# Kernel tuning notes

Hardware: AMD Instinct MI355X
Metric: run time of the kernel (lower is better)

Reference implementation:

```python
import jax, jax.numpy as jnp
import numpy as np
from functools import partial

EPS = 1e-5
PATCH = 3
STYLE_STRENGTH = 1.0


def _whiten_color_mats(x):
    # x: (b, c, n) already flattened; returns mean, eigvecs, eigvals of covariance
    mean = x.mean(axis=-1, keepdims=True)
    xc = x - mean
    n = x.shape[-1]
    cov = jnp.einsum('bcn,bdn->bcd', xc, xc) / (n - 1)
    evals, evecs = jnp.linalg.eigh(cov)
    evals = jnp.maximum(evals, EPS)
    return mean, xc, evecs, evals


def whitening(x):
    b, c, h, w = x.shape
    xf = x.reshape(b, c, h * w)
    _, xc, E, d = _whiten_color_mats(xf)
    # W = E diag(d^-1/2) E^T
    Wm = jnp.einsum('bce,be,bde->bcd', E, d ** -0.5, E)
    return jnp.einsum('bcd,bdn->bcn', Wm, xc).reshape(b, c, h, w)


def coloring(x, style):
    b, c, h, w = x.shape
    xf = x.reshape(b, c, h * w)
    sf = style.reshape(b, c, -1)
    smean, sc, E, d = _whiten_color_mats(sf)
    Cm = jnp.einsum('bce,be,bde->bcd', E, d ** 0.5, E)
    out = jnp.einsum('bcd,bdn->bcn', Cm, xf) + smean
    return out.reshape(b, c, h, w)


def extract_style_kernels(style):
    # returns (b, hw, c, 3, 3) patches and (b, hw, 1, 1, 1) L2 norms
    b, c, H, W = style.shape
    p = jnp.pad(style, ((0, 0), (0, 0), (1, 1), (1, 1)), mode='reflect')
    patches = jnp.stack([p[:, :, i:i + H, j:j + W]
                         for i in range(PATCH) for j in range(PATCH)], axis=-1)  # (b,c,H,W,9)
    k = patches.reshape(b, c, H * W, PATCH * PATCH).transpose(0, 2, 1, 3)  # (b,hw,c,9)
    norm = jnp.sqrt(jnp.sum(k * k, axis=(2, 3))) + EPS  # (b,hw)
    return k.reshape(b, H * W, c, PATCH, PATCH), norm[:, :, None, None, None]


_DN = ('NCHW', 'OIHW', 'NCHW')


def _conv_per_sample(feat, kern):
    # feat (c,H,W), kern (o,c,3,3): reflect-pad 1, VALID conv -> (o,H,W)
    fp = jnp.pad(feat, ((0, 0), (1, 1), (1, 1)), mode='reflect')
    out = jax.lax.conv_general_dilated(fp[None], kern, (1, 1), 'VALID',
                                       dimension_numbers=_DN)
    return out[0]


def _deconv_per_sample(onehot, kern):
    # conv_transpose2d(stride=1, padding=2) == VALID conv with flipped, transposed kernel
    kt = jnp.flip(kern, axis=(-2, -1)).transpose(1, 0, 2, 3)  # (c, hw, 3, 3)
    fp = jnp.pad(onehot, ((0, 0), (1, 1), (1, 1)), mode='reflect')
    out = jax.lax.conv_general_dilated(fp[None], kt, (1, 1), 'VALID',
                                       dimension_numbers=_DN)
    return out[0]


def norm_deconvolution(h, w, patch_size):
    full = np.zeros((h + patch_size - 1, w + patch_size - 1), dtype=np.float32)
    for x in range(patch_size):
        for y in range(patch_size):
            full[y:y + h, x:x + w] += 1.0
    pw = (patch_size - 1) // 2
    if pw > 0:
        full = full[pw:-pw, pw:-pw]
    return jnp.asarray(full)[None, None]  # (1,1,h,w)


def reassemble_feature(nc, ns):
    b, c, H, W = nc.shape
    hw = H * W
    kern, norm = extract_style_kernels(ns)
    score = jax.vmap(_conv_per_sample)(nc, kern / norm)  # (b, hw, H, W)
    idx = jnp.argmax(score, axis=1)  # (b, H, W)
    onehot = (jnp.arange(hw, dtype=idx.dtype)[None, :, None, None] == idx[:, None]
              ).astype(nc.dtype)  # (b, hw, H, W)
    recon = jax.vmap(_deconv_per_sample)(onehot, kern)  # (b, c, H, W)
    return recon / norm_deconvolution(H, W, PATCH).astype(recon.dtype)


def setup_inputs() -> dict:
    key = jax.random.key(0)
    k1, k2 = jax.random.split(key)
    content_feature = jax.random.normal(k1, (2, 256, 64, 64), dtype=jnp.float32)
    style_feature = jax.random.normal(k2, (2, 256, 64, 64), dtype=jnp.float32)
    return {"content_feature": content_feature, "style_feature": style_feature}


def reference(content_feature, style_feature):
    nc = whitening(content_feature)
    ns = whitening(style_feature)
    reassembled = reassemble_feature(nc, ns)
    stylized = coloring(reassembled, style_feature)
    return (1.0 - STYLE_STRENGTH) * content_feature + STYLE_STRENGTH * stylized
```

## Files before the change

kernel.cpp:

```cpp
#include <hip/hip_runtime.h>
#include <hip/hip_bf16.h>

#define C_ 256
#define N_ 4096
#define CN (C_*N_)
#define EPSF 1e-5f
#define NS_ITERS 6
#define KSPLIT 16
#define LSTR 40

typedef _Float16 f16x8 __attribute__((ext_vector_type(8)));
typedef float f32x4 __attribute__((ext_vector_type(4)));

__device__ __forceinline__ int refl(int t) {
  return t < 0 ? -t : (t > 63 ? 126 - t : t);
}

__device__ __forceinline__ unsigned short f2h(float x) {
  _Float16 h = (_Float16)x;
  return __builtin_bit_cast(unsigned short, h);
}
__device__ __forceinline__ float h2f(unsigned short u) {
  return (float)__builtin_bit_cast(_Float16, u);
}

__device__ __forceinline__ void fma16(float acc[4][4], float a0, float a1, float a2, float a3, float4 b) {
  acc[0][0] += a0*b.x; acc[0][1] += a0*b.y; acc[0][2] += a0*b.z; acc[0][3] += a0*b.w;
  acc[1][0] += a1*b.x; acc[1][1] += a1*b.y; acc[1][2] += a1*b.z; acc[1][3] += a1*b.w;
  acc[2][0] += a2*b.x; acc[2][1] += a2*b.y; acc[2][2] += a2*b.z; acc[2][3] += a2*b.w;
  acc[3][0] += a3*b.x; acc[3][1] += a3*b.y; acc[3][2] += a3*b.z; acc[3][3] += a3*b.w;
}

__device__ __forceinline__ void mm64_3term(unsigned short* sm, const float* A, const float* B,
                                           int m0, int n0, f32x4 acc[2][2]) {
  const int P = 64*LSTR;
  int t = threadIdx.x;
  int lane = t & 63;
  int wv = (t >> 7) & 1, wu = (t >> 6) & 1;
  int lx16 = lane & 15, quad = lane >> 4;
  int srow = t >> 2, sseg = (t & 3) * 8;
#pragma unroll
  for (int i = 0; i < 2; i++)
#pragma unroll
    for (int j = 0; j < 2; j++) acc[i][j] = (f32x4){0.f, 0.f, 0.f, 0.f};
  for (int k0 = 0; k0 < 256; k0 += 32) {
    __syncthreads();
    {
      const float* pa = &A[(size_t)(m0 + srow)*256 + k0 + sseg];
      const float* pb = &B[(size_t)(n0 + srow)*256 + k0 + sseg];
#pragma unroll
      for (int g = 0; g < 2; g++) {
        float4 va = *(const float4*)(pa + g*4);
        float4 vb = *(const float4*)(pb + g*4);
        float fa[4] = {va.x, va.y, va.z, va.w};
        float fb[4] = {vb.x, vb.y, vb.z, vb.w};
        unsigned short ha[4], la[4], hb[4], lb[4];
#pragma unroll
        for (int j = 0; j < 4; j++) {
          unsigned short h = f2h(fa[j]); ha[j] = h; la[j] = f2h(fa[j] - h2f(h));
          h = f2h(fb[j]); hb[j] = h; lb[j] = f2h(fb[j] - h2f(h));
        }
        int lo_ = srow*LSTR + sseg + g*4;
        *(ushort4*)&sm[0*P + lo_] = make_ushort4(ha[0], ha[1], ha[2], ha[3]);
        *(ushort4*)&sm[1*P + lo_] = make_ushort4(la[0], la[1], la[2], la[3]);
        *(ushort4*)&sm[2*P + lo_] = make_ushort4(hb[0], hb[1], hb[2], hb[3]);
        *(ushort4*)&sm[3*P + lo_] = make_ushort4(lb[0], lb[1], lb[2], lb[3]);
      }
    }
    __syncthreads();
    f16x8 ah[2], al[2], bh[2], bl[2];
#pragma unroll
    for (int mt = 0; mt < 2; mt++) {
      int arow = (wv*32 + mt*16 + lx16)*LSTR + quad*8;
      ah[mt] = *(const f16x8*)&sm[0*P + arow];
      al[mt] = *(const f16x8*)&sm[1*P + arow];
    }
#pragma unroll
    for (int nt = 0; nt < 2; nt++) {
      int brow = (wu*32 + nt*16 + lx16)*LSTR + quad*8;
      bh[nt] = *(const f16x8*)&sm[2*P + brow];
      bl[nt] = *(const f16x8*)&sm[3*P + brow];
    }
#pragma unroll
    for (int mt = 0; mt < 2; mt++)
#pragma unroll
      for (int nt = 0; nt < 2; nt++) {
        f32x4 a = acc[mt][nt];
        a = __builtin_amdgcn_mfma_f32_16x16x32_f16(ah[mt], bh[nt], a, 0, 0, 0);
        a = __builtin_amdgcn_mfma_f32_16x16x32_f16(ah[mt], bl[nt], a, 0, 0, 0);
        a = __builtin_amdgcn_mfma_f32_16x16x32_f16(al[mt], bh[nt], a, 0, 0, 0);
        acc[mt][nt] = a;
      }
  }
}

__global__ __launch_bounds__(256) void k_mean(const float* content, const float* style,
                                              float* means) {
  int c = blockIdx.x, m = blockIdx.y, t = threadIdx.x;
  const float* x = (m < 2 ? content : style) + (size_t)(m & 1) * CN + (size_t)c * N_;
  float s = 0.f;
  for (int i = t; i < N_; i += 256) s += x[i];
  __shared__ float red[256];
  red[t] = s; __syncthreads();
  for (int off = 128; off > 0; off >>= 1) { if (t < off) red[t] += red[t + off]; __syncthreads(); }
  if (t == 0) means[m * C_ + c] = red[0] * (1.f / N_);
}

__global__ __launch_bounds__(256) void k_splitcov(const float* content, const float* style,
                                                  unsigned short* sp) {
  int m = blockIdx.y;
  const float* x = (m < 2 ? content : style) + (size_t)(m & 1) * CN;
  size_t base = (size_t)m * 2 * (size_t)CN;
  size_t i = ((size_t)blockIdx.x * 256 + threadIdx.x) * 4;
  float4 v = *(const float4*)&x[i];
  float vv[4] = {v.x, v.y, v.z, v.w};
  unsigned short h[4], lo[4];
#pragma unroll
  for (int j = 0; j < 4; j++) {
    unsigned short hh = f2h(vv[j]);
    float r1 = vv[j] - h2f(hh);
    h[j] = hh; lo[j] = f2h(r1);
  }
  *(ushort4*)&sp[base + i]      = make_ushort4(h[0], h[1], h[2], h[3]);
  *(ushort4*)&sp[base + CN + i] = make_ushort4(lo[0], lo[1], lo[2], lo[3]);
}

__global__ __launch_bounds__(512) void k_covmm(const unsigned short* sp, float* covp) {
  __shared__ unsigned short sm[4*128*LSTR];
  const int P = 128*LSTR;
  int t = threadIdx.x;
  int kc = blockIdx.x, m = blockIdx.z;
  int ti = blockIdx.y >> 1, tj = blockIdx.y & 1;
  const unsigned short* Xh = sp + (size_t)m * 2 * (size_t)CN;
  const unsigned short* Xl = Xh + CN;
  int v0 = ti * 128, u0 = tj * 128;
  int wave = t >> 6, lane = t & 63;
  int wv = wave >> 1, wu = wave & 1;
  int lx16 = lane & 15, quad = lane >> 4;
  int srow = t >> 2, sseg = (t & 3) * 8;
  f32x4 acc[2][4];
#pragma unroll
  for (int i = 0; i < 2; i++)
#pragma unroll
    for (int j = 0; j < 4; j++) acc[i][j] = (f32x4){0.f, 0.f, 0.f, 0.f};

  int kbeg = kc * (N_ / KSPLIT), kend = kbeg + (N_ / KSPLIT);
  for (int k0 = kbeg; k0 < kend; k0 += 32) {
    __syncthreads();
    {
      size_t goA = (size_t)(v0 + srow) * N_ + k0 + sseg;
      size_t goB = (size_t)(u0 + srow) * N_ + k0 + sseg;
      int lo_ = srow * LSTR + sseg;
      *(float4*)&sm[0*P + lo_] = *(const float4*)&Xh[goA];
      *(float4*)&sm[1*P + lo_] = *(const float4*)&Xl[goA];
      *(float4*)&sm[2*P + lo_] = *(const float4*)&Xh[goB];
      *(float4*)&sm[3*P + lo_] = *(const float4*)&Xl[goB];
    }
    __syncthreads();
#pragma unroll
    for (int mt = 0; mt < 2; mt++) {
      int arow = (wv*32 + mt*16 + lx16)*LSTR + quad*8;
      f16x8 ah = *(const f16x8*)&sm[0*P + arow];
      f16x8 al = *(const f16x8*)&sm[1*P + arow];
#pragma unroll
      for (int nt = 0; nt < 4; nt++) {
        int brow = (wu*64 + nt*16 + lx16)*LSTR + quad*8;
        f16x8 bh = *(const f16x8*)&sm[2*P + brow];
        f16x8 bl = *(const f16x8*)&sm[3*P + brow];
        f32x4 a = acc[mt][nt];
        a = __builtin_amdgcn_mfma_f32_16x16x32_f16(ah, bh, a, 0, 0, 0);
        a = __builtin_amdgcn_mfma_f32_16x16x32_f16(ah, bl, a, 0, 0, 0);
        a = __builtin_amdgcn_mfma_f32_16x16x32_f16(al, bh, a, 0, 0, 0);
        acc[mt][nt] = a;
      }
    }
  }
  float* O = covp + ((size_t)kc*4 + m) * 65536;
#pragma unroll
  for (int mt = 0; mt < 2; mt++)
#pragma unroll
    for (int nt = 0; nt < 4; nt++)
#pragma unroll
      for (int i = 0; i < 4; i++)
        O[(size_t)(v0 + wv*32 + mt*16 + quad*4 + i)*C_ + (u0 + wu*64 + nt*16 + lx16)] =
            acc[mt][nt][i];
}

__global__ __launch_bounds__(256) void k_trace2(const float* covp, const float* means,
                                                float* cnrm) {
  int m = blockIdx.x, t = threadIdx.x;
  float s = 0.f;
#pragma unroll
  for (int kc = 0; kc < KSPLIT; kc++)
    s += covp[((size_t)kc*4 + m)*65536 + (size_t)t*257];
  float mi = means[m*C_ + t];
  float d = (s - (float)N_*mi*mi) * (1.f/(float)(N_-1));
  __shared__ float red[256];
  red[t] = d; __syncthreads();
  for (int off = 128; off > 0; off >>= 1) { if (t < off) red[t] += red[t + off]; __syncthreads(); }
  if (!t) cnrm[m] = red[0] * (1.3f/256.f);
}

__global__ __launch_bounds__(256) void k_covred_init(const float* covp, const float* means,
                                                     const float* cnrm, float* Y, float* Z) {
  int i = blockIdx.x, m = blockIdx.y, j = threadIdx.x;
  float s = 0.f;
#pragma unroll
  for (int kc = 0; kc < KSPLIT; kc++)
    s += covp[((size_t)kc*4 + m)*65536 + (size_t)i*C_ + j];
  float mi = means[m*C_ + i], mj = means[m*C_ + j];
  float cv = (s - (float)N_*mi*mj) * (1.f/(float)(N_-1));
  size_t o = (size_t)m*65536 + (size_t)i*C_ + j;
  Y[o] = cv / cnrm[m];
  Z[o] = (i == j) ? 1.f : 0.f;
}

__global__ __launch_bounds__(256) void k_nsA(const float* Zin, const float* Yin, float* T) {
  __shared__ unsigned short sm[4*64*LSTR];
  int m = blockIdx.y;
  int m0 = (blockIdx.x >> 2) * 64, n0 = (blockIdx.x & 3) * 64;
  const float* A = Zin + (size_t)m*65536;
  const float* B = Yin + (size_t)m*65536;
  float* O = T + (size_t)m*65536;
  f32x4 acc[2][2];
  mm64_3term(sm, A, B, m0, n0, acc);
  int t = threadIdx.x, lane = t & 63;
  int wv = (t >> 7) & 1, wu = (t >> 6) & 1, lx16 = lane & 15, quad = lane >> 4;
#pragma unroll
  for (int mt = 0; mt < 2; mt++)
#pragma unroll
    for (int nt = 0; nt < 2; nt++)
#pragma unroll
      for (int i = 0; i < 4; i++) {
        int r = m0 + wv*32 + mt*16 + quad*4 + i;
        int c = n0 + wu*32 + nt*16 + lx16;
        float v = acc[mt][nt][i];
        O[(size_t)r*256 + c] = (r == c) ? 3.f - v : -v;
      }
}

__global__ __launch_bounds__(256) void k_nsB(const float* Yin, const float* Zin, const float* T,
                                             float* Yout, float* Zout) {
  __shared__ unsigned short sm[4*64*LSTR];
  int m = blockIdx.y, z = blockIdx.z;
  const float* A = (z == 0 ? Yin : Zin) + (size_t)m*65536;
  const float* B = T + (size_t)m*65536;
  float* O = (z == 0 ? Yout : Zout) + (size_t)m*65536;
  int m0 = (blockIdx.x >> 2) * 64, n0 = (blockIdx.x & 3) * 64;
  f32x4 acc[2][2];
  mm64_3term(sm, A, B, m0, n0, acc);
  int t = threadIdx.x, lane = t & 63;
  int wv = (t >> 7) & 1, wu = (t >> 6) & 1, lx16 = lane & 15, quad = lane >> 4;
#pragma unroll
  for (int mt = 0; mt < 2; mt++)
#pragma unroll
    for (int nt = 0; nt < 2; nt++)
#pragma unroll
      for (int i = 0; i < 4; i++) {
        int r = m0 + wv*32 + mt*16 + quad*4 + i;
        int c = n0 + wu*32 + nt*16 + lx16;
        O[(size_t)r*256 + c] = 0.5f * acc[mt][nt][i];
      }
}

__global__ __launch_bounds__(256) void k_whiten(const float* content, const float* style,
                                                const float* Zall, const float* means,
                                                const float* cnrm, float* nc, float* ns) {
  int m = blockIdx.z;
  const float* x = (m < 2 ? content : style) + (size_t)(m & 1) * CN;
  float* outp = (m < 2 ? nc : ns) + (size_t)(m & 1) * CN;
  const float* Zm = Zall + (size_t)m*65536;
  const float* mean = means + m*C_;
  __shared__ float As[16][68], Bs[16][64];
  int t = threadIdx.x, tx = t & 15, ty = t >> 4;
  int n0 = blockIdx.x * 64, m0 = blockIdx.y * 64;
  float acc[4][4] = {};
  for (int k0 = 0; k0 < 256; k0 += 16) {
#pragma unroll
    for (int l = 0; l < 4; l++) {
      int e = t + l*256;
      { int kk = e & 15, mm = e >> 4; As[kk][mm] = Zm[(size_t)(m0+mm)*256 + k0+kk]; }
      { int nn = e & 63, kk = e >> 6;
        Bs[kk][nn] = x[(size_t)(k0+kk)*N_ + n0+nn] - mean[k0+kk]; }
    }
    __syncthreads();
#pragma unroll
    for (int kk = 0; kk < 16; kk++) {
      float4 b = *(const float4*)&Bs[kk][tx*4];
      fma16(acc, As[kk][ty*4+0], As[kk][ty*4+1], As[kk][ty*4+2], As[kk][ty*4+3], b);
    }
    __syncthreads();
  }
  float scale = 1.0f / sqrtf(cnrm[m]);
#pragma unroll
  for (int i = 0; i < 4; i++) {
    float4 o = make_float4(acc[i][0]*scale, acc[i][1]*scale, acc[i][2]*scale, acc[i][3]*scale);
    *(float4*)&outp[(size_t)(m0+ty*4+i)*N_ + n0 + tx*4] = o;
  }
}

__global__ __launch_bounds__(256) void k_ssq(const float* ns, float* ssq) {
  int b = blockIdx.y; int p = blockIdx.x * 256 + threadIdx.x;
  float acc = 0.f;
  for (int c = 0; c < C_; c++) { float v = ns[(size_t)b*CN + (size_t)c*N_ + p]; acc += v*v; }
  ssq[b*N_ + p] = acc;
}

__global__ __launch_bounds__(256) void k_rnorm(const float* ssq, float* rnorm) {
  int b = blockIdx.y; int s = blockIdx.x * 256 + threadIdx.x;
  int sy = s >> 6, sx = s & 63;
  float sum = 0.f;
#pragma unroll
  for (int ky = 0; ky < 3; ky++)
#pragma unroll
    for (int kx = 0; kx < 3; kx++)
      sum += ssq[b*N_ + refl(sy+ky-1)*64 + refl(sx+kx-1)];
  rnorm[b*N_ + s] = 1.f / (sqrtf(sum) + EPSF);
}

__global__ __launch_bounds__(256) void k_split(const float* nc_b, const float* ns_b,
                                               unsigned short* ncTh, unsigned short* ncTl,
                                               unsigned short* nsTh, unsigned short* nsTl) {
  int w = blockIdx.z;
  const float* src = w ? ns_b : nc_b;
  unsigned short* dh = w ? nsTh : ncTh;
  unsigned short* dl = w ? nsTl : ncTl;
  int u0 = blockIdx.x * 32, c0 = blockIdx.y * 32;
  __shared__ float tile[32][33];
  int t = threadIdx.x;
#pragma unroll
  for (int l = 0; l < 4; l++) {
    int e = t + l*256; int cc = e >> 5, uu = e & 31;
    tile[cc][uu] = src[(size_t)(c0+cc)*N_ + u0+uu];
  }
  __syncthreads();
#pragma unroll
  for (int l = 0; l < 4; l++) {
    int e = t + l*256; int uu = e >> 5, cc = e & 31;
    float v = tile[cc][uu];
    unsigned short h = f2h(v);
    float r1 = v - h2f(h);
    unsigned short lo = f2h(r1);
    size_t o = (size_t)(u0+uu)*C_ + c0+cc;
    dh[o] = h; dl[o] = lo;
  }
}

__global__ __launch_bounds__(512) void k_gram(const unsigned short* Ah_g, const unsigned short* Al_g,
                                              const unsigned short* Bh_g, const unsigned short* Bl_g,
                                              float* Hx) {
  __shared__ unsigned short sm[4*128*LSTR];
  const int P = 128*LSTR;
  int t = threadIdx.x;
  int v0 = blockIdx.y * 128, u0 = blockIdx.x * 128;
  int wave = t >> 6, lane = t & 63;
  int wv = wave >> 1, wu = wave & 1;
  int lx16 = lane & 15, quad = lane >> 4;
  int srow = t >> 2, sseg = (t & 3) * 8;
  f32x4 acc[2][4];
#pragma unroll
  for (int i = 0; i < 2; i++)
#pragma unroll
    for (int j = 0; j < 4; j++) acc[i][j] = (f32x4){0.f, 0.f, 0.f, 0.f};

  for (int k0 = 0; k0 < 256; k0 += 32) {
    __syncthreads();
    {
      size_t goA = (size_t)(v0 + srow)*C_ + k0 + sseg;
      size_t goB = (size_t)(u0 + srow)*C_ + k0 + sseg;
      int lo_ = srow*LSTR + sseg;
      *(float4*)&sm[0*P + lo_] = *(const float4*)&Ah_g[goA];
      *(float4*)&sm[1*P + lo_] = *(const float4*)&Al_g[goA];
      *(float4*)&sm[2*P + lo_] = *(const float4*)&Bh_g[goB];
      *(float4*)&sm[3*P + lo_] = *(const float4*)&Bl_g[goB];
    }
    __syncthreads();
    int kb = quad*8;
    f16x8 ah[2], al[2];
#pragma unroll
    for (int mt = 0; mt < 2; mt++) {
      int arow = (wv*32 + mt*16 + lx16)*LSTR + kb;
      ah[mt] = *(const f16x8*)&sm[0*P + arow];
      al[mt] = *(const f16x8*)&sm[1*P + arow];
    }
    f16x8 bh[4], bl[4];
#pragma unroll
    for (int nt = 0; nt < 4; nt++) {
      int brow = (wu*64 + nt*16 + lx16)*LSTR + kb;
      bh[nt] = *(const f16x8*)&sm[2*P + brow];
      bl[nt] = *(const f16x8*)&sm[3*P + brow];
    }
#pragma unroll
    for (int mt = 0; mt < 2; mt++)
#pragma unroll
      for (int nt = 0; nt < 4; nt++) {
        f32x4 a = acc[mt][nt];
        a = __builtin_amdgcn_mfma_f32_16x16x32_f16(ah[mt], bh[nt], a, 0, 0, 0);
        a = __builtin_amdgcn_mfma_f32_16x16x32_f16(ah[mt], bl[nt], a, 0, 0, 0);
        a = __builtin_amdgcn_mfma_f32_16x16x32_f16(al[mt], bh[nt], a, 0, 0, 0);
        acc[mt][nt] = a;
      }
  }
  float* Gs = (float*)sm;
  int btx = t & 15, bty = t >> 4;
#pragma unroll
  for (int h = 0; h < 2; h++) {
    __syncthreads();
    if ((wv >> 1) == h) {
      int rbase = (wv & 1) * 32;
#pragma unroll
      for (int mt = 0; mt < 2; mt++)
#pragma unroll
        for (int nt = 0; nt < 4; nt++)
#pragma unroll
          for (int i = 0; i < 4; i++)
            Gs[(rbase + mt*16 + quad*4 + i)*133 + wu*64 + nt*16 + lx16] = acc[mt][nt][i];
    }
    __syncthreads();
#pragma unroll
    for (int i = 0; i < 2; i++) {
      int px = bty*2 + i;
      int xm = refl(px-1), xp = refl(px+1);
#pragma unroll
      for (int jh = 0; jh < 2; jh++) {
        int ub = jh*64;
        float tmp[4];
#pragma unroll
        for (int j = 0; j < 4; j++) {
          int sx = btx*4 + j;
          int smm = refl(sx-1), sp = refl(sx+1);
          tmp[j] = Gs[xm*133 + ub + smm] + Gs[px*133 + ub + sx] + Gs[xp*133 + ub + sp];
        }
        *(float4*)&Hx[(size_t)(v0 + h*64 + px)*N_ + u0 + ub + btx*4] =
            make_float4(tmp[0], tmp[1], tmp[2], tmp[3]);
      }
    }
  }
}

__global__ __launch_bounds__(256) void k_argmax(const float* Hx, const float* rnorm,
                                                int* idx, int b) {
  int p = blockIdx.x, t = threadIdx.x;
  int py = p >> 6, px = p & 63;
  size_t r0 = (size_t)(refl(py-1)*64 + px) * N_;
  size_t r1 = (size_t)p * N_;
  size_t r2 = (size_t)(refl(py+1)*64 + px) * N_;
  float bv = -1e30f; int bs = 0;
  for (int s = t; s < N_; s += 256) {
    int sy = s >> 6, sx = s & 63;
    int u0 = refl(sy-1)*64 + sx, u2 = refl(sy+1)*64 + sx;
    float acc = Hx[r0 + u0] + Hx[r1 + s] + Hx[r2 + u2];
    float sc = acc * rnorm[b*N_ + s];
    if (sc > bv) { bv = sc; bs = s; }
  }
  __shared__ float sv[256]; __shared__ int si[256];
  sv[t] = bv; si[t] = bs; __syncthreads();
  for (int off = 128; off > 0; off >>= 1) {
    if (t < off) {
      if (sv[t+off] > sv[t] || (sv[t+off] == sv[t] && si[t+off] < si[t])) {
        sv[t] = sv[t+off]; si[t] = si[t+off];
      }
    }
    __syncthreads();
  }
  if (!t) idx[b*N_ + p] = si[0];
}

__global__ __launch_bounds__(256) void k_recon(const unsigned short* nsTh,
                                               const unsigned short* nsTl,
                                               const int* idx_b, float* recont_b) {
  int p = blockIdx.x, c = threadIdx.x;
  int py = p >> 6, px = p & 63;
  float acc = 0.f;
#pragma unroll
  for (int dy = 0; dy < 3; dy++)
#pragma unroll
    for (int dx = 0; dx < 3; dx++) {
      int q = refl(py+dy-1)*64 + refl(px+dx-1);
      int s = idx_b[q];
      int sy = s >> 6, sx = s & 63;
      size_t o = (size_t)(refl(sy+1-dy)*64 + refl(sx+1-dx))*C_ + c;
      acc += h2f(nsTh[o]) + h2f(nsTl[o]);
    }
  float dc = ((py==0||py==63)?2.f:3.f) * ((px==0||px==63)?2.f:3.f);
  recont_b[(size_t)p*C_ + c] = acc / dc;
}

__global__ __launch_bounds__(256) void k_color(const float* Yall, const float* recont_all,
                                               const float* cnrm, const float* means,
                                               float* out_all) {
  __shared__ unsigned short sm[4*64*LSTR];
  int b = blockIdx.z;
  const float* Ym = Yall + (size_t)(2+b)*65536;
  const float* recont = recont_all + (size_t)b*CN;
  const float* smean = means + (2+b)*C_;
  float* out = out_all + (size_t)b*CN;
  int m0 = blockIdx.y * 64;
  int n0 = blockIdx.x * 64;
  f32x4 acc[2][2];
  mm64_3term(sm, Ym, recont, m0, n0, acc);
  float scale = sqrtf(cnrm[2+b]);
  int t = threadIdx.x, lane = t & 63;
  int wv = (t >> 7) & 1, wu = (t >> 6) & 1, lx16 = lane & 15, quad = lane >> 4;
#pragma unroll
  for (int mt = 0; mt < 2; mt++)
#pragma unroll
    for (int nt = 0; nt < 2; nt++)
#pragma unroll
      for (int i = 0; i < 4; i++) {
        int r = m0 + wv*32 + mt*16 + quad*4 + i;
        int c = n0 + wu*32 + nt*16 + lx16;
        out[(size_t)r*N_ + c] = acc[mt][nt][i]*scale + smean[r];
      }
}

extern "C" void kernel_launch(void* const* d_in, const int* in_sizes, int n_in,
                              void* d_out, int out_size, void* d_ws, size_t ws_size,
                              hipStream_t stream) {
  const float* content = (const float*)d_in[0];
  const float* style   = (const float*)d_in[1];
  float* out = (float*)d_out;

  float* F = (float*)d_ws;
  float* means  = F + 0;
  float* cnrm   = F + 1024;
  float* Y      = F + 264192;
  float* Z      = F + 526336;
  float* Y2     = F + 788480;
  float* Z2     = F + 1050624;
  float* T      = F + 1312768;
  float* nc     = F + 1574912;
  float* ns     = F + 3672064;
  float* nstslot= F + 5769216;
  float* recont = F + 7866368;
  float* ssq    = F + 9963520;
  float* rnorm  = F + 9971712;
  int*   idx    = (int*)(F + 9979904);
  float* Hx     = F + 9988096;

  unsigned short* covsp = (unsigned short*)Hx;
  float* covp = Hx + 2*(size_t)CN*2;

  unsigned short* nsTh = (unsigned short*)nstslot;
  unsigned short* nsTl = (unsigned short*)nstslot + (size_t)CN;
  unsigned short* ncTh = (unsigned short*)nstslot + 2*(size_t)CN;
  unsigned short* ncTl = (unsigned short*)nstslot + 3*(size_t)CN;

  k_mean<<<dim3(256,4), 256, 0, stream>>>(content, style, means);
  k_splitcov<<<dim3(1024,4), 256, 0, stream>>>(content, style, covsp);
  k_covmm<<<dim3(KSPLIT,4,4), 512, 0, stream>>>(covsp, covp);
  k_trace2<<<4, 256, 0, stream>>>(covp, means, cnrm);
  k_covred_init<<<dim3(256,4), 256, 0, stream>>>(covp, means, cnrm, Y, Z);
  float *Ya = Y, *Za = Z, *Yb = Y2, *Zb = Z2;
  for (int it = 0; it < NS_ITERS; it++) {
    k_nsA<<<dim3(16,4), 256, 0, stream>>>(Za, Ya, T);
    k_nsB<<<dim3(16,4,2), 256, 0, stream>>>(Ya, Za, T, Yb, Zb);
    float* tmp;
    tmp = Ya; Ya = Yb; Yb = tmp;
    tmp = Za; Za = Zb; Zb = tmp;
  }
  k_whiten<<<dim3(64,4,4), 256, 0, stream>>>(content, style, Za, means, cnrm, nc, ns);
  k_ssq<<<dim3(16,2), 256, 0, stream>>>(ns, ssq);
  k_rnorm<<<dim3(16,2), 256, 0, stream>>>(ssq, rnorm);
  for (int b = 0; b < 2; b++) {
    k_split<<<dim3(128,8,2), 256, 0, stream>>>(nc + (size_t)b*CN, ns + (size_t)b*CN,
                                               ncTh, ncTl, nsTh, nsTl);
    k_gram<<<dim3(32,32), 512, 0, stream>>>(ncTh, ncTl, nsTh, nsTl, Hx);
    k_argmax<<<4096, 256, 0, stream>>>(Hx, rnorm, idx, b);
    k_recon<<<4096, 256, 0, stream>>>(nsTh, nsTl, idx + (size_t)b*N_,
                                      recont + (size_t)b*CN);
  }
  k_color<<<dim3(64,4,2), 256, 0, stream>>>(Ya, recont, cnrm, means, out);
}
```

Before: 404.0 us.

## Whiten with split-fp16 MFMA directly into transposed layout, dropping per-batch split pass

Fuses the fp16 hi/lo split of the inputs with a transposed, mean-centred copy in a single pass. The whitening matmul now runs on MFMA with three-term split precision and writes whitened features already in the transposed hi/lo layout that the gram and recon kernels consume. This removes the fp32 nc/ns round trip and the per-batch k_split launches. The sum-of-squares pass now reads the split layout. The cost is extra global writes in the first pass and some rounding from the fp16 hi/lo representation of the whitened output.

New measurement: 376.2 us. -6.9%, faster.

```diff
diff --git a/kernel.cpp b/kernel.cpp
--- a/kernel.cpp
+++ b/kernel.cpp
@@ -22,13 +22,6 @@
 }
 __device__ __forceinline__ float h2f(unsigned short u) {
   return (float)__builtin_bit_cast(_Float16, u);
-}
-
-__device__ __forceinline__ void fma16(float acc[4][4], float a0, float a1, float a2, float a3, float4 b) {
-  acc[0][0] += a0*b.x; acc[0][1] += a0*b.y; acc[0][2] += a0*b.z; acc[0][3] += a0*b.w;
-  acc[1][0] += a1*b.x; acc[1][1] += a1*b.y; acc[1][2] += a1*b.z; acc[1][3] += a1*b.w;
-  acc[2][0] += a2*b.x; acc[2][1] += a2*b.y; acc[2][2] += a2*b.z; acc[2][3] += a2*b.w;
-  acc[3][0] += a3*b.x; acc[3][1] += a3*b.y; acc[3][2] += a3*b.z; acc[3][3] += a3*b.w;
 }
 
 __device__ __forceinline__ void mm64_3term(unsigned short* sm, const float* A, const float* B,
@@ -106,23 +99,47 @@
   if (t == 0) means[m * C_ + c] = red[0] * (1.f / N_);
 }
 
-__global__ __launch_bounds__(256) void k_splitcov(const float* content, const float* style,
-                                                  unsigned short* sp) {
-  int m = blockIdx.y;
+__global__ __launch_bounds__(256) void k_splitall(const float* content, const float* style,
+                                                  const float* means,
+                                                  unsigned short* covsp, unsigned short* xcT) {
+  int m = blockIdx.z;
   const float* x = (m < 2 ? content : style) + (size_t)(m & 1) * CN;
-  size_t base = (size_t)m * 2 * (size_t)CN;
-  size_t i = ((size_t)blockIdx.x * 256 + threadIdx.x) * 4;
-  float4 v = *(const float4*)&x[i];
-  float vv[4] = {v.x, v.y, v.z, v.w};
-  unsigned short h[4], lo[4];
-#pragma unroll
-  for (int j = 0; j < 4; j++) {
-    unsigned short hh = f2h(vv[j]);
-    float r1 = vv[j] - h2f(hh);
-    h[j] = hh; lo[j] = f2h(r1);
-  }
-  *(ushort4*)&sp[base + i]      = make_ushort4(h[0], h[1], h[2], h[3]);
-  *(ushort4*)&sp[base + CN + i] = make_ushort4(lo[0], lo[1], lo[2], lo[3]);
+  int u0 = blockIdx.x * 32, c0 = blockIdx.y * 32;
+  unsigned short* ch_ = covsp + (size_t)(2*m+0)*CN;
+  unsigned short* cl_ = covsp + (size_t)(2*m+1)*CN;
+  unsigned short* th_ = xcT + (size_t)(2*m+0)*CN;
+  unsigned short* tl_ = xcT + (size_t)(2*m+1)*CN;
+  __shared__ float tile[32][33];
+  int t = threadIdx.x;
+  {
+    int cc = t >> 3, uu4 = (t & 7) * 4;
+    float4 v = *(const float4*)&x[(size_t)(c0+cc)*N_ + u0 + uu4];
+    float f[4] = {v.x, v.y, v.z, v.w};
+    unsigned short h[4], lo[4];
+#pragma unroll
+    for (int j = 0; j < 4; j++) {
+      unsigned short hh = f2h(f[j]);
+      h[j] = hh; lo[j] = f2h(f[j] - h2f(hh));
+      tile[cc][uu4+j] = f[j];
+    }
+    size_t o = (size_t)(c0+cc)*N_ + u0 + uu4;
+    *(ushort4*)&ch_[o] = make_ushort4(h[0], h[1], h[2], h[3]);
+    *(ushort4*)&cl_[o] = make_ushort4(lo[0], lo[1], lo[2], lo[3]);
+  }
+  __syncthreads();
+  {
+    int uu = t >> 3, cc4 = (t & 7) * 4;
+    unsigned short h[4], lo[4];
+#pragma unroll
+    for (int j = 0; j < 4; j++) {
+      float v = tile[cc4+j][uu] - means[m*C_ + c0 + cc4 + j];
+      unsigned short hh = f2h(v);
+      h[j] = hh; lo[j] = f2h(v - h2f(hh));
+    }
+    size_t o = (size_t)(u0+uu)*C_ + c0 + cc4;
+    *(ushort4*)&th_[o] = make_ushort4(h[0], h[1], h[2], h[3]);
+    *(ushort4*)&tl_[o] = make_ushort4(lo[0], lo[1], lo[2], lo[3]);
+  }
 }
 
 __global__ __launch_bounds__(512) void k_covmm(const unsigned short* sp, float* covp) {
@@ -263,46 +280,113 @@
       }
 }
 
-__global__ __launch_bounds__(256) void k_whiten(const float* content, const float* style,
-                                                const float* Zall, const float* means,
-                                                const float* cnrm, float* nc, float* ns) {
+__global__ __launch_bounds__(256) void k_whitenT(const unsigned short* xcT, const float* Zall,
+                                                 const float* cnrm, unsigned short* outT) {
+  __shared__ unsigned short sm[4*64*LSTR];
+  const int P = 64*LSTR;
   int m = blockIdx.z;
-  const float* x = (m < 2 ? content : style) + (size_t)(m & 1) * CN;
-  float* outp = (m < 2 ? nc : ns) + (size_t)(m & 1) * CN;
+  int v0 = blockIdx.x * 64, c0 = blockIdx.y * 64;
   const float* Zm = Zall + (size_t)m*65536;
-  const float* mean = means + m*C_;
-  __shared__ float As[16][68], Bs[16][64];
-  int t = threadIdx.x, tx = t & 15, ty = t >> 4;
-  int n0 = blockIdx.x * 64, m0 = blockIdx.y * 64;
-  float acc[4][4] = {};
-  for (int k0 = 0; k0 < 256; k0 += 16) {
-#pragma unroll
-    for (int l = 0; l < 4; l++) {
-      int e = t + l*256;
-      { int kk = e & 15, mm = e >> 4; As[kk][mm] = Zm[(size_t)(m0+mm)*256 + k0+kk]; }
-      { int nn = e & 63, kk = e >> 6;
-        Bs[kk][nn] = x[(size_t)(k0+kk)*N_ + n0+nn] - mean[k0+kk]; }
-    }
-    __syncthreads();
-#pragma unroll
-    for (int kk = 0; kk < 16; kk++) {
-      float4 b = *(const float4*)&Bs[kk][tx*4];
-      fma16(acc, As[kk][ty*4+0], As[kk][ty*4+1], As[kk][ty*4+2], As[kk][ty*4+3], b);
-    }
-    __syncthreads();
+  const unsigned short* Bh_g = xcT + (size_t)(2*m+0)*CN;
+  const unsigned short* Bl_g = xcT + (size_t)(2*m+1)*CN;
+  unsigned short* Oh = outT + (size_t)(2*m+0)*CN;
+  unsigned short* Ol = outT + (size_t)(2*m+1)*CN;
+  int t = threadIdx.x, lane = t & 63;
+  int wv = (t >> 7) & 1, wu = (t >> 6) & 1;
+  int lx16 = lane & 15, quad = lane >> 4;
+  int srow = t >> 2, sseg = (t & 3) * 8;
+  f32x4 acc[2][2];
+#pragma unroll
+  for (int i = 0; i < 2; i++)
+#pragma unroll
+    for (int j = 0; j < 2; j++) acc[i][j] = (f32x4){0.f, 0.f, 0.f, 0.f};
+  for (int k0 = 0; k0 < 256; k0 += 32) {
+    __syncthreads();
+    {
+      const float* pa = &Zm[(size_t)(c0 + srow)*256 + k0 + sseg];
+      int lo_ = srow*LSTR + sseg;
+#pragma unroll
+      for (int g = 0; g < 2; g++) {
+        float4 va = *(const float4*)(pa + g*4);
+        float fa[4] = {va.x, va.y, va.z, va.w};
+        unsigned short ha[4], la[4];
+#pragma unroll
+        for (int j = 0; j < 4; j++) {
+          unsigned short h = f2h(fa[j]); ha[j] = h; la[j] = f2h(fa[j] - h2f(h));
+        }
+        *(ushort4*)&sm[0*P + lo_ + g*4] = make_ushort4(ha[0], ha[1], ha[2], ha[3]);
+        *(ushort4*)&sm[1*P + lo_ + g*4] = make_ushort4(la[0], la[1], la[2], la[3]);
+      }
+      size_t gb = (size_t)(v0 + srow)*C_ + k0 + sseg;
+      *(float4*)&sm[2*P + lo_] = *(const float4*)&Bh_g[gb];
+      *(float4*)&sm[3*P + lo_] = *(const float4*)&Bl_g[gb];
+    }
+    __syncthreads();
+    f16x8 ah[2], al[2], bh[2], bl[2];
+#pragma unroll
+    for (int mt = 0; mt < 2; mt++) {
+      int arow = (wv*32 + mt*16 + lx16)*LSTR + quad*8;
+      ah[mt] = *(const f16x8*)&sm[0*P + arow];
+      al[mt] = *(const f16x8*)&sm[1*P + arow];
+    }
+#pragma unroll
+    for (int nt = 0; nt < 2; nt++) {
+      int brow = (wu*32 + nt*16 + lx16)*LSTR + quad*8;
+      bh[nt] = *(const f16x8*)&sm[2*P + brow];
+      bl[nt] = *(const f16x8*)&sm[3*P + brow];
+    }
+#pragma unroll
+    for (int mt = 0; mt < 2; mt++)
+#pragma unroll
+      for (int nt = 0; nt < 2; nt++) {
+        f32x4 a = acc[mt][nt];
+        a = __builtin_amdgcn_mfma_f32_16x16x32_f16(ah[mt], bh[nt], a, 0, 0, 0);
+        a = __builtin_amdgcn_mfma_f32_16x16x32_f16(ah[mt], bl[nt], a, 0, 0, 0);
+        a = __builtin_amdgcn_mfma_f32_16x16x32_f16(al[mt], bh[nt], a, 0, 0, 0);
+        acc[mt][nt] = a;
+      }
   }
   float scale = 1.0f / sqrtf(cnrm[m]);
-#pragma unroll
-  for (int i = 0; i < 4; i++) {
-    float4 o = make_float4(acc[i][0]*scale, acc[i][1]*scale, acc[i][2]*scale, acc[i][3]*scale);
-    *(float4*)&outp[(size_t)(m0+ty*4+i)*N_ + n0 + tx*4] = o;
-  }
-}
-
-__global__ __launch_bounds__(256) void k_ssq(const float* ns, float* ssq) {
+  __syncthreads();
+  unsigned short* Th = sm;
+  unsigned short* Tl = sm + 64*72;
+#pragma unroll
+  for (int mt = 0; mt < 2; mt++)
+#pragma unroll
+    for (int nt = 0; nt < 2; nt++)
+#pragma unroll
+      for (int i = 0; i < 4; i++) {
+        int chl = wv*32 + mt*16 + quad*4 + i;
+        int vl  = wu*32 + nt*16 + lx16;
+        float w = acc[mt][nt][i] * scale;
+        unsigned short h = f2h(w);
+        unsigned short l = f2h(w - h2f(h));
+        Th[vl*72 + chl] = h;
+        Tl[vl*72 + chl] = l;
+      }
+  __syncthreads();
+  int vr = t >> 2, cs = (t & 3) * 16;
+  size_t go = (size_t)(v0 + vr)*C_ + c0 + cs;
+  *(float4*)&Oh[go]     = *(float4*)&Th[vr*72 + cs];
+  *(float4*)&Oh[go + 8] = *(float4*)&Th[vr*72 + cs + 8];
+  *(float4*)&Ol[go]     = *(float4*)&Tl[vr*72 + cs];
+  *(float4*)&Ol[go + 8] = *(float4*)&Tl[vr*72 + cs + 8];
+}
+
+__global__ __launch_bounds__(256) void k_ssq(const unsigned short* outT, float* ssq) {
   int b = blockIdx.y; int p = blockIdx.x * 256 + threadIdx.x;
+  const unsigned short* h = outT + (size_t)(2*(2+b))*CN + (size_t)p*C_;
+  const unsigned short* l = h + CN;
   float acc = 0.f;
-  for (int c = 0; c < C_; c++) { float v = ns[(size_t)b*CN + (size_t)c*N_ + p]; acc += v*v; }
+  for (int c = 0; c < C_; c += 4) {
+    ushort4 hv = *(const ushort4*)&h[c];
+    ushort4 lv = *(const ushort4*)&l[c];
+    float v0 = h2f(hv.x) + h2f(lv.x);
+    float v1 = h2f(hv.y) + h2f(lv.y);
+    float v2 = h2f(hv.z) + h2f(lv.z);
+    float v3 = h2f(hv.w) + h2f(lv.w);
+    acc += v0*v0 + v1*v1 + v2*v2 + v3*v3;
+  }
   ssq[b*N_ + p] = acc;
 }
 
@@ -316,34 +400,6 @@
     for (int kx = 0; kx < 3; kx++)
       sum += ssq[b*N_ + refl(sy+ky-1)*64 + refl(sx+kx-1)];
   rnorm[b*N_ + s] = 1.f / (sqrtf(sum) + EPSF);
-}
-
-__global__ __launch_bounds__(256) void k_split(const float* nc_b, const float* ns_b,
-                                               unsigned short* ncTh, unsigned short* ncTl,
-                                               unsigned short* nsTh, unsigned short* nsTl) {
-  int w = blockIdx.z;
-  const float* src = w ? ns_b : nc_b;
-  unsigned short* dh = w ? nsTh : ncTh;
-  unsigned short* dl = w ? nsTl : ncTl;
-  int u0 = blockIdx.x * 32, c0 = blockIdx.y * 32;
-  __shared__ float tile[32][33];
-  int t = threadIdx.x;
-#pragma unroll
-  for (int l = 0; l < 4; l++) {
-    int e = t + l*256; int cc = e >> 5, uu = e & 31;
-    tile[cc][uu] = src[(size_t)(c0+cc)*N_ + u0+uu];
-  }
-  __syncthreads();
-#pragma unroll
-  for (int l = 0; l < 4; l++) {
-    int e = t + l*256; int uu = e >> 5, cc = e & 31;
-    float v = tile[cc][uu];
-    unsigned short h = f2h(v);
-    float r1 = v - h2f(h);
-    unsigned short lo = f2h(r1);
-    size_t o = (size_t)(u0+uu)*C_ + c0+cc;
-    dh[o] = h; dl[o] = lo;
-  }
 }
 
 __global__ __launch_bounds__(512) void k_gram(const unsigned short* Ah_g, const unsigned short* Al_g,
@@ -529,9 +585,8 @@
   float* Y2     = F + 788480;
   float* Z2     = F + 1050624;
   float* T      = F + 1312768;
-  float* nc     = F + 1574912;
-  float* ns     = F + 3672064;
-  float* nstslot= F + 5769216;
+  float* ncreg  = F + 1574912;
+  float* nsreg  = F + 3672064;
   float* recont = F + 7866368;
   float* ssq    = F + 9963520;
   float* rnorm  = F + 9971712;
@@ -539,15 +594,13 @@
   float* Hx     = F + 9988096;
 
   unsigned short* covsp = (unsigned short*)Hx;
-  float* covp = Hx + 2*(size_t)CN*2;
-
-  unsigned short* nsTh = (unsigned short*)nstslot;
-  unsigned short* nsTl = (unsigned short*)nstslot + (size_t)CN;
-  unsigned short* ncTh = (unsigned short*)nstslot + 2*(size_t)CN;
-  unsigned short* ncTl = (unsigned short*)nstslot + 3*(size_t)CN;
+  float* covp = Hx + 4194304;
+
+  unsigned short* xcT  = (unsigned short*)nsreg;
+  unsigned short* outT = (unsigned short*)ncreg;
 
   k_mean<<<dim3(256,4), 256, 0, stream>>>(content, style, means);
-  k_splitcov<<<dim3(1024,4), 256, 0, stream>>>(content, style, covsp);
+  k_splitall<<<dim3(128,8,4), 256, 0, stream>>>(content, style, means, covsp, xcT);
   k_covmm<<<dim3(KSPLIT,4,4), 512, 0, stream>>>(covsp, covp);
   k_trace2<<<4, 256, 0, stream>>>(covp, means, cnrm);
   k_covred_init<<<dim3(256,4), 256, 0, stream>>>(covp, means, cnrm, Y, Z);
@@ -559,16 +612,18 @@
     tmp = Ya; Ya = Yb; Yb = tmp;
     tmp = Za; Za = Zb; Zb = tmp;
   }
-  k_whiten<<<dim3(64,4,4), 256, 0, stream>>>(content, style, Za, means, cnrm, nc, ns);
-  k_ssq<<<dim3(16,2), 256, 0, stream>>>(ns, ssq);
+  k_whitenT<<<dim3(64,4,4), 256, 0, stream>>>(xcT, Za, cnrm, outT);
+  k_ssq<<<dim3(16,2), 256, 0, stream>>>(outT, ssq);
   k_rnorm<<<dim3(16,2), 256, 0, stream>>>(ssq, rnorm);
   for (int b = 0; b < 2; b++) {
-    k_split<<<dim3(128,8,2), 256, 0, stream>>>(nc + (size_t)b*CN, ns + (size_t)b*CN,
-                                               ncTh, ncTl, nsTh, nsTl);
-    k_gram<<<dim3(32,32), 512, 0, stream>>>(ncTh, ncTl, nsTh, nsTl, Hx);
+    k_gram<<<dim3(32,32), 512, 0, stream>>>(outT + (size_t)(2*b)*CN,
+                                            outT + (size_t)(2*b+1)*CN,
+                                            outT + (size_t)(2*(2+b))*CN,
+                                            outT + (size_t)(2*(2+b)+1)*CN, Hx);
     k_argmax<<<4096, 256, 0, stream>>>(Hx, rnorm, idx, b);
-    k_recon<<<4096, 256, 0, stream>>>(nsTh, nsTl, idx + (size_t)b*N_,
-                                      recont + (size_t)b*CN);
+    k_recon<<<4096, 256, 0, stream>>>(outT + (size_t)(2*(2+b))*CN,
+                                      outT + (size_t)(2*(2+b)+1)*CN,
+                                      idx + (size_t)b*N_, recont + (size_t)b*CN);
   }
   k_color<<<dim3(64,4,2), 256, 0, stream>>>(Ya, recont, cnrm, means, out);
 }
```
